# Optimization experiments

Measured on AMD Instinct MI355X. Metric: run time of the kernel, lower is better.

## Reference

```python
import jax, jax.numpy as jnp
import numpy as np

D_MODEL = 1024
N_HEADS = 16
D_HEAD = D_MODEL // N_HEADS


def setup_inputs() -> dict:
    key = jax.random.key(0)
    ks = jax.random.split(key, 9)
    B, S = 2, 2048
    s = 0.02
    return {
        "x": jax.random.normal(ks[0], (B, S, D_MODEL), dtype=jnp.float32),
        "Wq": jax.random.normal(ks[1], (D_MODEL, D_MODEL), dtype=jnp.float32) * s,
        "bq": jnp.zeros((D_MODEL,), dtype=jnp.float32),
        "Wk": jax.random.normal(ks[2], (D_MODEL, D_MODEL), dtype=jnp.float32) * s,
        "bk": jnp.zeros((D_MODEL,), dtype=jnp.float32),
        "Wv": jax.random.normal(ks[3], (D_MODEL, D_MODEL), dtype=jnp.float32) * s,
        "bv": jnp.zeros((D_MODEL,), dtype=jnp.float32),
        "Wo": jax.random.normal(ks[4], (D_MODEL, D_MODEL), dtype=jnp.float32) * s,
        "bo": jnp.zeros((D_MODEL,), dtype=jnp.float32),
    }


def reference(x, Wq, bq, Wk, bk, Wv, bv, Wo, bo):
    B, S, _ = x.shape
    # projections -> [B, H, S, Dh]
    def split_heads(t):
        return t.reshape(B, S, N_HEADS, D_HEAD).transpose(0, 2, 1, 3)
    Q = split_heads(x @ Wq + bq)
    K = split_heads(x @ Wk + bk)
    V = split_heads(x @ Wv + bv)
    scores = jnp.einsum('bhqd,bhkd->bhqk', Q, K)  # [B,H,S,S]
    mask = jnp.tril(jnp.ones((S, S), dtype=bool))
    # NB: original masks BEFORE scaling (mask fill -1e9 then /sqrt(d_head))
    scores = jnp.where(mask[None, None], scores, jnp.float32(-1e9))
    scores = scores / jnp.sqrt(jnp.float32(D_HEAD))
    attn = jax.nn.softmax(scores, axis=-1)
    ctx = jnp.einsum('bhqk,bhkd->bhqd', attn, V)
    ctx = ctx.transpose(0, 2, 1, 3).reshape(B, S, D_MODEL)
    return ctx @ Wo + bo
```

## Files before the change

### kernel.cpp

```cpp
#include <hip/hip_runtime.h>

typedef __bf16 bf16;
typedef __bf16 bf16x8 __attribute__((ext_vector_type(8)));
typedef __bf16 bf16x4 __attribute__((ext_vector_type(4)));
typedef float  f32x4  __attribute__((ext_vector_type(4)));

#define D_MODEL 1024
#define S_LEN   2048
#define NHEAD   16
#define DHEAD   64
#define BATCH   2
#define MROWS   (BATCH * S_LEN)

#define QSCALE 0.18033688011112042f

__device__ __forceinline__ void gld_lds16(const void* g, void* lds_base) {
    __builtin_amdgcn_global_load_lds(
        (const __attribute__((address_space(1))) void*)g,
        (__attribute__((address_space(3))) void*)lds_base, 16, 0, 0);
}

__global__ void prep_kernel(const float* __restrict__ x,
                            const float* __restrict__ W0, const float* __restrict__ W1,
                            const float* __restrict__ W2, const float* __restrict__ W3,
                            bf16* __restrict__ xb, bf16* __restrict__ Wt) {
    int tx = threadIdx.x, ty = threadIdx.y;
    if (blockIdx.z == 4) {
        int tid = ty * 32 + tx;
        size_t base = ((size_t)blockIdx.y * 32 + blockIdx.x) * 4096;
#pragma unroll
        for (int j = 0; j < 4; j++) {
            size_t i = base + (size_t)(j * 256 + tid) * 4;
            f32x4 v = *(const f32x4*)(x + i);
            bf16x4 o;
            o[0] = (bf16)v[0]; o[1] = (bf16)v[1]; o[2] = (bf16)v[2]; o[3] = (bf16)v[3];
            *(bf16x4*)(xb + i) = o;
        }
        return;
    }
    __shared__ float tile[32][33];
    const float* W = (blockIdx.z == 0) ? W0 : (blockIdx.z == 1) ? W1
                   : (blockIdx.z == 2) ? W2 : W3;
    int n0 = blockIdx.x * 32, k0 = blockIdx.y * 32;
#pragma unroll
    for (int j = 0; j < 4; j++)
        tile[ty + 8 * j][tx] = W[(size_t)(k0 + ty + 8 * j) * D_MODEL + n0 + tx];
    __syncthreads();
    bf16* out = Wt + (size_t)blockIdx.z * D_MODEL * D_MODEL;
#pragma unroll
    for (int j = 0; j < 4; j++)
        out[(size_t)(n0 + ty + 8 * j) * D_MODEL + k0 + tx] = (bf16)tile[tx][ty + 8 * j];
}

template <int MODE>
__global__ __launch_bounds__(256, 2) void gemm_kernel(
    const bf16* __restrict__ A, const bf16* __restrict__ Bt,
    const float* __restrict__ b0, const float* __restrict__ b1, const float* __restrict__ b2,
    bf16* __restrict__ Qo, bf16* __restrict__ Ko, bf16* __restrict__ Vto,
    float* __restrict__ Co) {
    __shared__ bf16 sA[128 * 32];
    __shared__ bf16 sB[128 * 32];
    const int t = threadIdx.x;
    const int wave = t >> 6, lane = t & 63;
    const int wm = wave >> 1, wn = wave & 1;
    const int quad = lane >> 4, m16 = lane & 15;
    const int row0 = blockIdx.y * 128, col0 = blockIdx.x * 128;
    const int K = D_MODEL;

    f32x4 acc[4][4];
#pragma unroll
    for (int i = 0; i < 4; i++)
#pragma unroll
        for (int j = 0; j < 4; j++) acc[i][j] = (f32x4){0.f, 0.f, 0.f, 0.f};

    for (int kk = 0; kk < K; kk += 32) {
#pragma unroll
        for (int i = 0; i < 2; i++) {
            int cb = i * 256 + wave * 64;
            int c  = cb + lane;
            int r  = c >> 2, kg = c & 3;
            gld_lds16(A  + (size_t)(row0 + r) * K + kk + kg * 8, (char*)sA + cb * 16);
            gld_lds16(Bt + (size_t)(col0 + r) * K + kk + kg * 8, (char*)sB + cb * 16);
        }
        __syncthreads();
        bf16x8 af[4], bfr[4];
#pragma unroll
        for (int mi = 0; mi < 4; mi++)
            af[mi] = *(const bf16x8*)&sA[(wm * 64 + mi * 16 + m16) * 32 + quad * 8];
#pragma unroll
        for (int ni = 0; ni < 4; ni++)
            bfr[ni] = *(const bf16x8*)&sB[(wn * 64 + ni * 16 + m16) * 32 + quad * 8];
#pragma unroll
        for (int mi = 0; mi < 4; mi++)
#pragma unroll
            for (int ni = 0; ni < 4; ni++)
                acc[mi][ni] = __builtin_amdgcn_mfma_f32_16x16x32_bf16(
                    af[mi], bfr[ni], acc[mi][ni], 0, 0, 0);
        __syncthreads();
    }

    if (MODE == 1) {
#pragma unroll
        for (int mi = 0; mi < 4; mi++) {
            int r0 = row0 + wm * 64 + mi * 16 + quad * 4;
#pragma unroll
            for (int ni = 0; ni < 4; ni++) {
                int col = col0 + wn * 64 + ni * 16 + m16;
                float bias = b0[col];
#pragma unroll
                for (int r = 0; r < 4; r++)
                    Co[(size_t)(r0 + r) * D_MODEL + col] = acc[mi][ni][r] + bias;
            }
        }
    } else {
        int sel = col0 >> 10;
        const float* bias_arr = (sel == 0) ? b0 : (sel == 1) ? b1 : b2;
#pragma unroll
        for (int mi = 0; mi < 4; mi++) {
            int s0g = row0 + wm * 64 + mi * 16 + quad * 4;
            int b = s0g >> 11, ss0 = s0g & 2047;
#pragma unroll
            for (int ni = 0; ni < 4; ni++) {
                int col = col0 + wn * 64 + ni * 16 + m16;
                int cn = col & 1023;
                int h = cn >> 6, d = cn & 63;
                float bias = bias_arr[cn];
                if (sel < 2) {
                    bf16* dst = (sel == 0) ? Qo : Ko;
                    float scl = (sel == 0) ? QSCALE : 1.0f;
                    size_t base = (((size_t)b * NHEAD + h) * S_LEN);
#pragma unroll
                    for (int r = 0; r < 4; r++)
                        dst[(base + ss0 + r) * DHEAD + d] = (bf16)((acc[mi][ni][r] + bias) * scl);
                } else {
                    bf16x4 pk;
#pragma unroll
                    for (int r = 0; r < 4; r++) pk[r] = (bf16)(acc[mi][ni][r] + bias);
                    *(bf16x4*)(Vto + (((size_t)b * NHEAD + h) * DHEAD + d) * S_LEN + ss0) = pk;
                }
            }
        }
    }
}

__global__ __launch_bounds__(256, 2) void attn_kernel(
    const bf16* __restrict__ Q, const bf16* __restrict__ K,
    const bf16* __restrict__ Vt, bf16* __restrict__ ctx) {
    __shared__ bf16 Kt_s[3][64 * 64];
    __shared__ bf16 Vt_s[3][64 * 64];

    const int t = threadIdx.x, wave = t >> 6, lane = t & 63;
    const int quad = lane >> 4, m16 = lane & 15;
    const int bh = blockIdx.y, p = blockIdx.x;
    const int tT[2] = {p, 31 - p};
    const int nt = 32 - p;
    const size_t base = (size_t)bh * S_LEN * DHEAD;

    bf16x8 aq[2][2];
#pragma unroll
    for (int it = 0; it < 2; it++)
#pragma unroll
        for (int kst = 0; kst < 2; kst++)
            aq[it][kst] = *(const bf16x8*)(Q + base
                + (size_t)(tT[it] * 64 + wave * 16 + m16) * DHEAD + kst * 32 + quad * 8);

    f32x4 o[2][4];
#pragma unroll
    for (int it = 0; it < 2; it++)
#pragma unroll
        for (int di = 0; di < 4; di++) o[it][di] = (f32x4){0.f, 0.f, 0.f, 0.f};
    float l_acc[2] = {0.f, 0.f};

    auto stage = [&](int j, int buf) {
#pragma unroll
        for (int i = 0; i < 2; i++) {
            int cb = i * 256 + wave * 64;
            int c  = cb + lane;
            int pos = c >> 3, g = c & 7;
            int gk = g ^ (pos & 7);
            gld_lds16(K  + base + (size_t)(j * 64 + pos) * DHEAD + gk * 8,
                      (char*)&Kt_s[buf][0] + cb * 16);
            gld_lds16(Vt + base + (size_t)pos * S_LEN + j * 64 + gk * 8,
                      (char*)&Vt_s[buf][0] + cb * 16);
        }
    };

    stage(0, 0);
    if (nt > 1) stage(1, 1);

    for (int j = 0; j < nt; ++j) {
        if (j + 1 < nt) asm volatile("s_waitcnt vmcnt(4)\n\ts_barrier" ::: "memory");
        else            asm volatile("s_waitcnt vmcnt(0)\n\ts_barrier" ::: "memory");
        if (j + 2 < nt) stage(j + 2, (j + 2) % 3);

        const int cur = j % 3;
        const bool aAct = (j <= tT[0]);
        const int kt0 = j * 64;

        auto computeTile = [&](bool both) {
            int itlo = both ? 0 : 1;
            f32x4 sc[2][4];
#pragma unroll
            for (int it = 0; it < 2; it++)
#pragma unroll
                for (int ni = 0; ni < 4; ni++) sc[it][ni] = (f32x4){0.f, 0.f, 0.f, 0.f};
            __builtin_amdgcn_s_setprio(1);
#pragma unroll
            for (int ni = 0; ni < 4; ni++) {
                int pos = ni * 16 + m16;
#pragma unroll
                for (int kst = 0; kst < 2; kst++) {
                    int gg = (kst * 4 + quad) ^ (pos & 7);
                    bf16x8 kf = *(const bf16x8*)&Kt_s[cur][pos * 64 + gg * 8];
                    sc[1][ni] = __builtin_amdgcn_mfma_f32_16x16x32_bf16(
                        kf, aq[1][kst], sc[1][ni], 0, 0, 0);
                    if (both)
                        sc[0][ni] = __builtin_amdgcn_mfma_f32_16x16x32_bf16(
                            kf, aq[0][kst], sc[0][ni], 0, 0, 0);
                }
            }
            __builtin_amdgcn_s_setprio(0);
#pragma unroll
            for (int it = 0; it < 2; it++) {
                if (it < itlo) continue;
                if (j == tT[it]) {
                    int qg = tT[it] * 64 + wave * 16 + m16;
#pragma unroll
                    for (int ni = 0; ni < 4; ni++)
#pragma unroll
                        for (int r = 0; r < 4; r++) {
                            int kp = kt0 + ni * 16 + quad * 4 + r;
                            if (kp > qg) sc[it][ni][r] = -1e9f;
                        }
                }
            }
            unsigned int pd[2][4][2];
#pragma unroll
            for (int it = 0; it < 2; it++) {
                if (it < itlo) continue;
                float ls0 = 0.f, ls1 = 0.f;
#pragma unroll
                for (int ni = 0; ni < 4; ni++) {
                    float p0 = __builtin_amdgcn_exp2f(sc[it][ni][0]);
                    float p1 = __builtin_amdgcn_exp2f(sc[it][ni][1]);
                    float p2 = __builtin_amdgcn_exp2f(sc[it][ni][2]);
                    float p3 = __builtin_amdgcn_exp2f(sc[it][ni][3]);
                    union { bf16x4 h; unsigned int u[2]; } cv;
                    cv.h[0] = (bf16)p0; cv.h[1] = (bf16)p1;
                    cv.h[2] = (bf16)p2; cv.h[3] = (bf16)p3;
                    pd[it][ni][0] = cv.u[0];
                    pd[it][ni][1] = cv.u[1];
                    ls0 += p0 + p1;
                    ls1 += p2 + p3;
                }
                l_acc[it] += ls0 + ls1;
            }
#pragma unroll
            for (int kst = 0; kst < 2; kst++) {
                bf16x8 ap[2];
#pragma unroll
                for (int it = 0; it < 2; it++) {
                    if (it < itlo) continue;
                    unsigned int x0 = pd[it][2 * kst][0],     y0 = pd[it][2 * kst][1];
                    unsigned int x1 = pd[it][2 * kst + 1][0], y1 = pd[it][2 * kst + 1][1];
                    asm("v_permlane32_swap_b32 %0, %1" : "+v"(x0), "+v"(x1));
                    asm("v_permlane32_swap_b32 %0, %1" : "+v"(y0), "+v"(y1));
                    asm("v_permlane16_swap_b32 %0, %1" : "+v"(x0), "+v"(x1));
                    asm("v_permlane16_swap_b32 %0, %1" : "+v"(y0), "+v"(y1));
                    union { unsigned int u[4]; bf16x8 v; } pk;
                    pk.u[0] = x0; pk.u[1] = y0; pk.u[2] = x1; pk.u[3] = y1;
                    ap[it] = pk.v;
                }
                __builtin_amdgcn_s_setprio(1);
#pragma unroll
                for (int di = 0; di < 4; di++) {
                    int d = di * 16 + m16;
                    int gg = (kst * 4 + quad) ^ (d & 7);
                    bf16x8 vf = *(const bf16x8*)&Vt_s[cur][d * 64 + gg * 8];
                    o[1][di] = __builtin_amdgcn_mfma_f32_16x16x32_bf16(
                        vf, ap[1], o[1][di], 0, 0, 0);
                    if (both)
                        o[0][di] = __builtin_amdgcn_mfma_f32_16x16x32_bf16(
                            vf, ap[0], o[0][di], 0, 0, 0);
                }
                __builtin_amdgcn_s_setprio(0);
            }
        };
        if (aAct) computeTile(true);
        else      computeTile(false);
    }

    int b = bh >> 4, h = bh & 15;
#pragma unroll
    for (int it = 0; it < 2; it++) {
        float l = l_acc[it];
        l += __shfl_xor(l, 16);
        l += __shfl_xor(l, 32);
        float rl = 1.0f / l;
        int s = tT[it] * 64 + wave * 16 + m16;
#pragma unroll
        for (int di = 0; di < 4; di++) {
            bf16x4 pk;
#pragma unroll
            for (int r = 0; r < 4; r++) pk[r] = (bf16)(o[it][di][r] * rl);
            *(bf16x4*)(ctx + ((size_t)b * S_LEN + s) * D_MODEL
                       + h * DHEAD + di * 16 + quad * 4) = pk;
        }
    }
}

extern "C" void kernel_launch(void* const* d_in, const int* in_sizes, int n_in,
                              void* d_out, int out_size, void* d_ws, size_t ws_size,
                              hipStream_t stream) {
    const float* x  = (const float*)d_in[0];
    const float* Wq = (const float*)d_in[1];
    const float* bq = (const float*)d_in[2];
    const float* Wk = (const float*)d_in[3];
    const float* bk = (const float*)d_in[4];
    const float* Wv = (const float*)d_in[5];
    const float* bv = (const float*)d_in[6];
    const float* Wo = (const float*)d_in[7];
    const float* bo = (const float*)d_in[8];
    float* out = (float*)d_out;

    char* ws = (char*)d_ws;
    const size_t MB = 1u << 20;
    bf16* xb  = (bf16*)(ws + 0);
    bf16* Wt  = (bf16*)(ws + 8  * MB);
    bf16* Qb  = (bf16*)(ws + 16 * MB);
    bf16* Kb  = (bf16*)(ws + 24 * MB);
    bf16* Vtb = (bf16*)(ws + 32 * MB);
    bf16* ctx = (bf16*)(ws + 0);

    prep_kernel<<<dim3(32, 32, 5), dim3(32, 8), 0, stream>>>(x, Wq, Wk, Wv, Wo, xb, Wt);
    gemm_kernel<0><<<dim3(24, 32), 256, 0, stream>>>(xb, Wt, bq, bk, bv,
                                                     Qb, Kb, Vtb, nullptr);
    attn_kernel<<<dim3(16, 32), 256, 0, stream>>>(Qb, Kb, Vtb, ctx);
    gemm_kernel<1><<<dim3(8, 32), 256, 0, stream>>>(ctx, Wt + 3 * 1024 * 1024,
                                                    bo, nullptr, nullptr,
                                                    nullptr, nullptr, nullptr, out);
}
```

Before: 190.2 us.

## Split paired query tiles into one tile per block with heaviest-first order

The attention kernel no longer pairs query tiles p and 31-p in one block. Each block now handles a single query tile, the grid is ordered so the longest causal tiles launch first, and launch bounds rise to 4 blocks per CU. K/V staging drops from triple to double buffering with a full vmcnt(0) wait each iteration, which shrinks LDS and registers per block. In exchange, every K/V tile is loaded once per query tile instead of being shared by two, and less load latency is hidden behind compute.

```diff
diff --git a/kernel.cpp b/kernel.cpp
--- a/kernel.cpp
+++ b/kernel.cpp
@@ -143,33 +143,29 @@
     }
 }
 
-__global__ __launch_bounds__(256, 2) void attn_kernel(
+__global__ __launch_bounds__(256, 4) void attn_kernel(
     const bf16* __restrict__ Q, const bf16* __restrict__ K,
     const bf16* __restrict__ Vt, bf16* __restrict__ ctx) {
-    __shared__ bf16 Kt_s[3][64 * 64];
-    __shared__ bf16 Vt_s[3][64 * 64];
+    __shared__ bf16 Kt_s[2][64 * 64];
+    __shared__ bf16 Vt_s[2][64 * 64];
 
     const int t = threadIdx.x, wave = t >> 6, lane = t & 63;
     const int quad = lane >> 4, m16 = lane & 15;
-    const int bh = blockIdx.y, p = blockIdx.x;
-    const int tT[2] = {p, 31 - p};
-    const int nt = 32 - p;
+    const int bh = blockIdx.x;
+    const int qt = 31 - blockIdx.y;
+    const int nt = qt + 1;
     const size_t base = (size_t)bh * S_LEN * DHEAD;
 
-    bf16x8 aq[2][2];
-#pragma unroll
-    for (int it = 0; it < 2; it++)
-#pragma unroll
-        for (int kst = 0; kst < 2; kst++)
-            aq[it][kst] = *(const bf16x8*)(Q + base
-                + (size_t)(tT[it] * 64 + wave * 16 + m16) * DHEAD + kst * 32 + quad * 8);
-
-    f32x4 o[2][4];
-#pragma unroll
-    for (int it = 0; it < 2; it++)
-#pragma unroll
-        for (int di = 0; di < 4; di++) o[it][di] = (f32x4){0.f, 0.f, 0.f, 0.f};
-    float l_acc[2] = {0.f, 0.f};
+    bf16x8 aq[2];
+#pragma unroll
+    for (int kst = 0; kst < 2; kst++)
+        aq[kst] = *(const bf16x8*)(Q + base
+            + (size_t)(qt * 64 + wave * 16 + m16) * DHEAD + kst * 32 + quad * 8);
+
+    f32x4 o[4];
+#pragma unroll
+    for (int di = 0; di < 4; di++) o[di] = (f32x4){0.f, 0.f, 0.f, 0.f};
+    float l_acc = 0.f;
 
     auto stage = [&](int j, int buf) {
 #pragma unroll
@@ -186,126 +182,99 @@
     };
 
     stage(0, 0);
-    if (nt > 1) stage(1, 1);
 
     for (int j = 0; j < nt; ++j) {
-        if (j + 1 < nt) asm volatile("s_waitcnt vmcnt(4)\n\ts_barrier" ::: "memory");
-        else            asm volatile("s_waitcnt vmcnt(0)\n\ts_barrier" ::: "memory");
-        if (j + 2 < nt) stage(j + 2, (j + 2) % 3);
-
-        const int cur = j % 3;
-        const bool aAct = (j <= tT[0]);
+        asm volatile("s_waitcnt vmcnt(0)\n\ts_barrier" ::: "memory");
+        if (j + 1 < nt) stage(j + 1, (j + 1) & 1);
+
+        const int cur = j & 1;
         const int kt0 = j * 64;
 
-        auto computeTile = [&](bool both) {
-            int itlo = both ? 0 : 1;
-            f32x4 sc[2][4];
-#pragma unroll
-            for (int it = 0; it < 2; it++)
-#pragma unroll
-                for (int ni = 0; ni < 4; ni++) sc[it][ni] = (f32x4){0.f, 0.f, 0.f, 0.f};
+        f32x4 sc[4];
+#pragma unroll
+        for (int ni = 0; ni < 4; ni++) sc[ni] = (f32x4){0.f, 0.f, 0.f, 0.f};
+        __builtin_amdgcn_s_setprio(1);
+#pragma unroll
+        for (int ni = 0; ni < 4; ni++) {
+            int pos = ni * 16 + m16;
+#pragma unroll
+            for (int kst = 0; kst < 2; kst++) {
+                int gg = (kst * 4 + quad) ^ (pos & 7);
+                bf16x8 kf = *(const bf16x8*)&Kt_s[cur][pos * 64 + gg * 8];
+                sc[ni] = __builtin_amdgcn_mfma_f32_16x16x32_bf16(
+                    kf, aq[kst], sc[ni], 0, 0, 0);
+            }
+        }
+        __builtin_amdgcn_s_setprio(0);
+
+        if (j == qt) {
+            int qg = qt * 64 + wave * 16 + m16;
+#pragma unroll
+            for (int ni = 0; ni < 4; ni++)
+#pragma unroll
+                for (int r = 0; r < 4; r++) {
+                    int kp = kt0 + ni * 16 + quad * 4 + r;
+                    if (kp > qg) sc[ni][r] = -1e9f;
+                }
+        }
+
+        unsigned int pd[4][2];
+        {
+            float ls0 = 0.f, ls1 = 0.f;
+#pragma unroll
+            for (int ni = 0; ni < 4; ni++) {
+                float p0 = __builtin_amdgcn_exp2f(sc[ni][0]);
+                float p1 = __builtin_amdgcn_exp2f(sc[ni][1]);
+                float p2 = __builtin_amdgcn_exp2f(sc[ni][2]);
+                float p3 = __builtin_amdgcn_exp2f(sc[ni][3]);
+                union { bf16x4 h; unsigned int u[2]; } cv;
+                cv.h[0] = (bf16)p0; cv.h[1] = (bf16)p1;
+                cv.h[2] = (bf16)p2; cv.h[3] = (bf16)p3;
+                pd[ni][0] = cv.u[0];
+                pd[ni][1] = cv.u[1];
+                ls0 += p0 + p1;
+                ls1 += p2 + p3;
+            }
+            l_acc += ls0 + ls1;
+        }
+
+#pragma unroll
+        for (int kst = 0; kst < 2; kst++) {
+            unsigned int x0 = pd[2 * kst][0],     y0 = pd[2 * kst][1];
+            unsigned int x1 = pd[2 * kst + 1][0], y1 = pd[2 * kst + 1][1];
+            asm("v_permlane32_swap_b32 %0, %1" : "+v"(x0), "+v"(x1));
+            asm("v_permlane32_swap_b32 %0, %1" : "+v"(y0), "+v"(y1));
+            asm("v_permlane16_swap_b32 %0, %1" : "+v"(x0), "+v"(x1));
+            asm("v_permlane16_swap_b32 %0, %1" : "+v"(y0), "+v"(y1));
+            union { unsigned int u[4]; bf16x8 v; } pk;
+            pk.u[0] = x0; pk.u[1] = y0; pk.u[2] = x1; pk.u[3] = y1;
+            bf16x8 ap = pk.v;
             __builtin_amdgcn_s_setprio(1);
 #pragma unroll
-            for (int ni = 0; ni < 4; ni++) {
-                int pos = ni * 16 + m16;
-#pragma unroll
-                for (int kst = 0; kst < 2; kst++) {
-                    int gg = (kst * 4 + quad) ^ (pos & 7);
-                    bf16x8 kf = *(const bf16x8*)&Kt_s[cur][pos * 64 + gg * 8];
-                    sc[1][ni] = __builtin_amdgcn_mfma_f32_16x16x32_bf16(
-                        kf, aq[1][kst], sc[1][ni], 0, 0, 0);
-                    if (both)
-                        sc[0][ni] = __builtin_amdgcn_mfma_f32_16x16x32_bf16(
-                            kf, aq[0][kst], sc[0][ni], 0, 0, 0);
-                }
+            for (int di = 0; di < 4; di++) {
+                int d = di * 16 + m16;
+                int gg = (kst * 4 + quad) ^ (d & 7);
+                bf16x8 vf = *(const bf16x8*)&Vt_s[cur][d * 64 + gg * 8];
+                o[di] = __builtin_amdgcn_mfma_f32_16x16x32_bf16(
+                    vf, ap, o[di], 0, 0, 0);
             }
             __builtin_amdgcn_s_setprio(0);
-#pragma unroll
-            for (int it = 0; it < 2; it++) {
-                if (it < itlo) continue;
-                if (j == tT[it]) {
-                    int qg = tT[it] * 64 + wave * 16 + m16;
-#pragma unroll
-                    for (int ni = 0; ni < 4; ni++)
-#pragma unroll
-                        for (int r = 0; r < 4; r++) {
-                            int kp = kt0 + ni * 16 + quad * 4 + r;
-                            if (kp > qg) sc[it][ni][r] = -1e9f;
-                        }
-                }
-            }
-            unsigned int pd[2][4][2];
-#pragma unroll
-            for (int it = 0; it < 2; it++) {
-                if (it < itlo) continue;
-                float ls0 = 0.f, ls1 = 0.f;
-#pragma unroll
-                for (int ni = 0; ni < 4; ni++) {
-                    float p0 = __builtin_amdgcn_exp2f(sc[it][ni][0]);
-                    float p1 = __builtin_amdgcn_exp2f(sc[it][ni][1]);
-                    float p2 = __builtin_amdgcn_exp2f(sc[it][ni][2]);
-                    float p3 = __builtin_amdgcn_exp2f(sc[it][ni][3]);
-                    union { bf16x4 h; unsigned int u[2]; } cv;
-                    cv.h[0] = (bf16)p0; cv.h[1] = (bf16)p1;
-                    cv.h[2] = (bf16)p2; cv.h[3] = (bf16)p3;
-                    pd[it][ni][0] = cv.u[0];
-                    pd[it][ni][1] = cv.u[1];
-                    ls0 += p0 + p1;
-                    ls1 += p2 + p3;
-                }
-                l_acc[it] += ls0 + ls1;
-            }
-#pragma unroll
-            for (int kst = 0; kst < 2; kst++) {
-                bf16x8 ap[2];
-#pragma unroll
-                for (int it = 0; it < 2; it++) {
-                    if (it < itlo) continue;
-                    unsigned int x0 = pd[it][2 * kst][0],     y0 = pd[it][2 * kst][1];
-                    unsigned int x1 = pd[it][2 * kst + 1][0], y1 = pd[it][2 * kst + 1][1];
-                    asm("v_permlane32_swap_b32 %0, %1" : "+v"(x0), "+v"(x1));
-                    asm("v_permlane32_swap_b32 %0, %1" : "+v"(y0), "+v"(y1));
-                    asm("v_permlane16_swap_b32 %0, %1" : "+v"(x0), "+v"(x1));
-                    asm("v_permlane16_swap_b32 %0, %1" : "+v"(y0), "+v"(y1));
-                    union { unsigned int u[4]; bf16x8 v; } pk;
-                    pk.u[0] = x0; pk.u[1] = y0; pk.u[2] = x1; pk.u[3] = y1;
-                    ap[it] = pk.v;
-                }
-                __builtin_amdgcn_s_setprio(1);
-#pragma unroll
-                for (int di = 0; di < 4; di++) {
-                    int d = di * 16 + m16;
-                    int gg = (kst * 4 + quad) ^ (d & 7);
-                    bf16x8 vf = *(const bf16x8*)&Vt_s[cur][d * 64 + gg * 8];
-                    o[1][di] = __builtin_amdgcn_mfma_f32_16x16x32_bf16(
-                        vf, ap[1], o[1][di], 0, 0, 0);
-                    if (both)
-                        o[0][di] = __builtin_amdgcn_mfma_f32_16x16x32_bf16(
-                            vf, ap[0], o[0][di], 0, 0, 0);
-                }
-                __builtin_amdgcn_s_setprio(0);
-            }
-        };
-        if (aAct) computeTile(true);
-        else      computeTile(false);
+        }
     }
 
     int b = bh >> 4, h = bh & 15;
-#pragma unroll
-    for (int it = 0; it < 2; it++) {
-        float l = l_acc[it];
-        l += __shfl_xor(l, 16);
-        l += __shfl_xor(l, 32);
-        float rl = 1.0f / l;
-        int s = tT[it] * 64 + wave * 16 + m16;
-#pragma unroll
-        for (int di = 0; di < 4; di++) {
-            bf16x4 pk;
-#pragma unroll
-            for (int r = 0; r < 4; r++) pk[r] = (bf16)(o[it][di][r] * rl);
-            *(bf16x4*)(ctx + ((size_t)b * S_LEN + s) * D_MODEL
-                       + h * DHEAD + di * 16 + quad * 4) = pk;
-        }
+    float l = l_acc;
+    l += __shfl_xor(l, 16);
+    l += __shfl_xor(l, 32);
+    float rl = 1.0f / l;
+    int s = qt * 64 + wave * 16 + m16;
+#pragma unroll
+    for (int di = 0; di < 4; di++) {
+        bf16x4 pk;
+#pragma unroll
+        for (int r = 0; r < 4; r++) pk[r] = (bf16)(o[di][r] * rl);
+        *(bf16x4*)(ctx + ((size_t)b * S_LEN + s) * D_MODEL
+                   + h * DHEAD + di * 16 + quad * 4) = pk;
     }
 }
 
@@ -335,7 +304,7 @@
     prep_kernel<<<dim3(32, 32, 5), dim3(32, 8), 0, stream>>>(x, Wq, Wk, Wv, Wo, xb, Wt);
     gemm_kernel<0><<<dim3(24, 32), 256, 0, stream>>>(xb, Wt, bq, bk, bv,
                                                      Qb, Kb, Vtb, nullptr);
-    attn_kernel<<<dim3(16, 32), 256, 0, stream>>>(Qb, Kb, Vtb, ctx);
+    attn_kernel<<<dim3(32, 32), 256, 0, stream>>>(Qb, Kb, Vtb, ctx);
     gemm_kernel<1><<<dim3(8, 32), 256, 0, stream>>>(ctx, Wt + 3 * 1024 * 1024,
                                                     bo, nullptr, nullptr,
                                                     nullptr, nullptr, nullptr, out);
```

New measurement: 181.9 us. 4.3% less time.
